# Kernel optimization log

Hardware: AMD Instinct MI355X
Metric: run time of the kernel (lower is better)

The kernel has to match this reference:

```python
import jax, jax.numpy as jnp
import numpy as np

N = 50_000       # nodes
E = 1_600_000    # edges (avg degree 32)
F_IN = 128       # input features
H = 32           # hidden channels (both GCNConv layers)
C = 16           # num classes


def setup_inputs() -> dict:
    key = jax.random.key(0)
    ks = jax.random.split(key, 6)
    x = jax.random.normal(ks[0], (N, F_IN), dtype=jnp.float32)
    edge_index = jax.random.randint(ks[1], (2, E), 0, N, dtype=jnp.int32)
    W1 = jax.random.normal(ks[2], (F_IN, H), dtype=jnp.float32) / np.float32(np.sqrt(F_IN))
    b1 = jnp.zeros((H,), jnp.float32)
    W2 = jax.random.normal(ks[3], (H, H), dtype=jnp.float32) / np.float32(np.sqrt(H))
    b2 = jnp.zeros((H,), jnp.float32)
    Wc = jax.random.normal(ks[4], (H, C), dtype=jnp.float32) / np.float32(np.sqrt(H))
    bc = jnp.zeros((C,), jnp.float32)
    return {"x": x, "edge_index": edge_index, "W1": W1, "b1": b1,
            "W2": W2, "b2": b2, "Wc": Wc, "bc": bc}


def _gcn_conv(x, W, b, src, dst, deg_inv_sqrt, n):
    """PyG GCNConv: xW, then D^{-1/2}(A+I)D^{-1/2} aggregation, then bias.

    src/dst already include self-loops; deg_inv_sqrt precomputed on dst.
    """
    xw = x @ W                                   # [N, H]
    norm = deg_inv_sqrt[src] * deg_inv_sqrt[dst]  # [E+N]
    msg = xw[src] * norm[:, None]                # gather + scale, [E+N, H]
    out = jax.ops.segment_sum(msg, dst, num_segments=n)  # scatter-add
    return out + b


def reference(x, edge_index, W1, b1, W2, b2, Wc, bc):
    n = x.shape[0]
    loops = jnp.arange(n, dtype=edge_index.dtype)
    src = jnp.concatenate([edge_index[0], loops])  # add self-loops
    dst = jnp.concatenate([edge_index[1], loops])
    # degree over destination column (edge weight 1), as PyG gcn_norm does
    deg = jax.ops.segment_sum(jnp.ones_like(dst, dtype=x.dtype), dst, num_segments=n)
    deg_inv_sqrt = jnp.where(deg > 0, jax.lax.rsqrt(deg), 0.0)

    h = jnp.tanh(_gcn_conv(x, W1, b1, src, dst, deg_inv_sqrt, n))
    h = jnp.tanh(_gcn_conv(h, W2, b2, src, dst, deg_inv_sqrt, n))
    out = h @ Wc + bc
    return (out, h)
```

## Files before the change

kernel.cpp:

```cpp
#include <hip/hip_runtime.h>
#include <hip/hip_bf16.h>

#define NN 50000
#define EE 1600000
#define FIN 128
#define HH 32
#define CC 16
#define NB 782
#define NBLK 782
#define CHUNK 2048
#define FCAP 3072

typedef unsigned short u16;
typedef unsigned int u32;
typedef unsigned char u8;

__device__ __forceinline__ float bf2f(u16 u) {
    union { u32 i; float f; } v; v.i = ((u32)u) << 16; return v.f;
}
__device__ __forceinline__ u16 f2bf(float f) {
    union { float f; u32 i; } v; v.f = f;
    u32 x = v.i;
    return (u16)((x + 0x7fffu + ((x >> 16) & 1u)) >> 16);
}

__global__ __launch_bounds__(256) void k_place(const int* __restrict__ src, const int* __restrict__ dst,
                                               int* __restrict__ locT,
                                               u16* __restrict__ gsrc, u8* __restrict__ grel) {
    __shared__ int dst_s[CHUNK];
    __shared__ u16 s_src[CHUNK];
    __shared__ u8  s_rel[CHUNK];
    __shared__ int cur[NB];
    __shared__ int ps[256];
    const int tid = threadIdx.x, blk = blockIdx.x;
    const int e0 = blk * CHUNK;
    int cnt = EE - e0; if (cnt > CHUNK) cnt = CHUNK;

    const uint4* gd4 = (const uint4*)(dst + e0);
    for (int i = tid; i < cnt / 4; i += 256) ((uint4*)dst_s)[i] = gd4[i];
    for (int i = tid; i < NB; i += 256) cur[i] = 0;
    __syncthreads();

    for (int k = 0; k < CHUNK / 256; ++k) {
        int i = k * 256 + tid;
        if (i < cnt) atomicAdd(&cur[dst_s[i] >> 6], 1);
    }
    __syncthreads();

    const int bi = tid * 4;
    int v0 = 0, v1 = 0, v2 = 0, v3 = 0;
    if (bi < NB)     v0 = cur[bi];
    if (bi + 1 < NB) v1 = cur[bi + 1];
    if (bi + 2 < NB) v2 = cur[bi + 2];
    if (bi + 3 < NB) v3 = cur[bi + 3];
    ps[tid] = v0 + v1 + v2 + v3;
    __syncthreads();
    for (int off = 1; off < 256; off <<= 1) {
        int t = (tid >= off) ? ps[tid - off] : 0;
        __syncthreads();
        ps[tid] += t;
        __syncthreads();
    }
    int run = (tid == 0) ? 0 : ps[tid - 1];
    if (bi < NB)     { cur[bi] = run;     locT[(size_t)bi * NBLK + blk] = run;       run += v0; }
    if (bi + 1 < NB) { cur[bi + 1] = run; locT[(size_t)(bi + 1) * NBLK + blk] = run; run += v1; }
    if (bi + 2 < NB) { cur[bi + 2] = run; locT[(size_t)(bi + 2) * NBLK + blk] = run; run += v2; }
    if (bi + 3 < NB) { cur[bi + 3] = run; locT[(size_t)(bi + 3) * NBLK + blk] = run; run += v3; }
    if (tid == 255) locT[(size_t)NB * NBLK + blk] = ps[255];
    __syncthreads();

    for (int k = 0; k < CHUNK / 256; ++k) {
        int i = k * 256 + tid;
        if (i < cnt) {
            int d = dst_s[i];
            int pos = atomicAdd(&cur[d >> 6], 1);
            s_src[pos] = (u16)src[e0 + i];
            s_rel[pos] = (u8)(d & 63);
        }
    }
    __syncthreads();

    const uint4* ss = (const uint4*)s_src;
    uint4* gs = (uint4*)(gsrc + (size_t)blk * CHUNK);
    for (int i = tid; i < (cnt * 2) / 16; i += 256) gs[i] = ss[i];
    const uint4* sr = (const uint4*)s_rel;
    uint4* gr = (uint4*)(grel + (size_t)blk * CHUNK);
    for (int i = tid; i < cnt / 16; i += 256) gr[i] = sr[i];
}

__global__ __launch_bounds__(256) void k_btot(const int* __restrict__ locT, int* __restrict__ btot) {
    __shared__ int ps[256];
    const int cb = blockIdx.x;
    int s = 0;
    for (int b = threadIdx.x; b < NBLK; b += 256)
        s += locT[(size_t)(cb + 1) * NBLK + b] - locT[(size_t)cb * NBLK + b];
    ps[threadIdx.x] = s;
    __syncthreads();
    for (int off = 128; off > 0; off >>= 1) {
        if (threadIdx.x < off) ps[threadIdx.x] += ps[threadIdx.x + off];
        __syncthreads();
    }
    if (threadIdx.x == 0) btot[cb] = ps[0];
}

__global__ __launch_bounds__(1024) void k_cscan(const int* __restrict__ btot, int* __restrict__ cbase,
                                                int* __restrict__ rowptr,
                                                const u32* __restrict__ xw_words, int* __restrict__ flag) {
    __shared__ int ps[1024];
    __shared__ int cs;
    const int t = threadIdx.x;
    if (t == 0) cs = 0;
    __syncthreads();
    if (t < 512) {
        float v = fabsf(bf2f((u16)(xw_words[t] & 0xffffu)));
        if (v >= 6.0e-8f && v <= 64.0f) atomicAdd(&cs, 1);
    }
    int myv = (t < NB) ? btot[t] : 0;
    ps[t] = myv;
    __syncthreads();
    for (int off = 1; off < 1024; off <<= 1) {
        int v = (t >= off) ? ps[t - off] : 0;
        __syncthreads();
        ps[t] += v;
        __syncthreads();
    }
    if (t < NB) cbase[t] = ps[t] - myv;
    if (t == 0) {
        cbase[NB] = EE; rowptr[NN] = EE;
        *flag = (cs > 384) ? 1 : 0;
    }
}

__global__ __launch_bounds__(256) void k_fine(const int* __restrict__ locT, const int* __restrict__ cbase,
                                              const u16* __restrict__ gsrc, const u8* __restrict__ grel,
                                              int* __restrict__ rowptr, float* __restrict__ dis,
                                              u16* __restrict__ entries) {
    __shared__ int beg_s[NBLK];
    __shared__ int fo[NBLK + 1];
    __shared__ int ps[256];
    __shared__ int h[64];
    __shared__ int cur[64];
    __shared__ u16 lsrc[FCAP];
    __shared__ u8  lrel[FCAP];
    __shared__ u16 lout[FCAP];
    const int tid = threadIdx.x, cb = blockIdx.x;

    for (int b = tid; b < NBLK; b += 256) {
        int beg = locT[(size_t)cb * NBLK + b];
        beg_s[b] = beg;
        fo[b] = locT[(size_t)(cb + 1) * NBLK + b] - beg;
    }
    if (tid < 64) h[tid] = 0;
    __syncthreads();

    const int b0 = tid * 4;
    int a0 = 0, a1 = 0, a2 = 0, a3 = 0;
    if (b0 < NBLK)     a0 = fo[b0];
    if (b0 + 1 < NBLK) a1 = fo[b0 + 1];
    if (b0 + 2 < NBLK) a2 = fo[b0 + 2];
    if (b0 + 3 < NBLK) a3 = fo[b0 + 3];
    ps[tid] = a0 + a1 + a2 + a3;
    __syncthreads();
    for (int off = 1; off < 256; off <<= 1) {
        int v = (tid >= off) ? ps[tid - off] : 0;
        __syncthreads();
        ps[tid] += v;
        __syncthreads();
    }
    int run = (tid == 0) ? 0 : ps[tid - 1];
    if (b0 < NBLK)     { fo[b0] = run;     run += a0; }
    if (b0 + 1 < NBLK) { fo[b0 + 1] = run; run += a1; }
    if (b0 + 2 < NBLK) { fo[b0 + 2] = run; run += a2; }
    if (b0 + 3 < NBLK) { fo[b0 + 3] = run; run += a3; }
    if (tid == 255) fo[NBLK] = ps[255];
    __syncthreads();
    const int T = fo[NBLK];
    const int base = cbase[cb];
    const bool staged = (T <= FCAP);

    if (staged) {
        for (int b = tid; b < NBLK; b += 256) {
            int g0 = b * CHUNK + beg_s[b];
            int o = fo[b];
            int L = fo[b + 1] - o;
            for (int j = 0; j < L; ++j) {
                u8 r = grel[g0 + j];
                lrel[o + j] = r;
                lsrc[o + j] = gsrc[g0 + j];
                atomicAdd(&h[r], 1);
            }
        }
    } else {
        for (int b = tid; b < NBLK; b += 256) {
            int g0 = b * CHUNK + beg_s[b];
            int L = fo[b + 1] - fo[b];
            for (int j = 0; j < L; ++j) atomicAdd(&h[grel[g0 + j]], 1);
        }
    }
    __syncthreads();

    int myv = (tid < 64) ? h[tid] : 0;
    ps[tid] = (tid < 64) ? myv : 0;
    __syncthreads();
    for (int off = 1; off < 64; off <<= 1) {
        int v = (tid >= off && tid < 64) ? ps[tid - off] : 0;
        __syncthreads();
        if (tid < 64) ps[tid] += v;
        __syncthreads();
    }
    if (tid < 64) {
        int excl = ps[tid] - myv;
        int n = cb * 64 + tid;
        cur[tid] = staged ? excl : base + excl;
        if (n < NN) {
            rowptr[n] = base + excl;
            dis[n] = rsqrtf((float)myv + 1.0f);
        }
    }
    __syncthreads();

    if (staged) {
        for (int i = tid; i < T; i += 256) {
            int pos = atomicAdd(&cur[lrel[i]], 1);
            lout[pos] = lsrc[i];
        }
        __syncthreads();
        for (int i = tid; i < T; i += 256) entries[base + i] = lout[i];
    } else {
        for (int b = tid; b < NBLK; b += 256) {
            int g0 = b * CHUNK + beg_s[b];
            int L = fo[b + 1] - fo[b];
            for (int j = 0; j < L; ++j) {
                int g = g0 + j;
                int pos = atomicAdd(&cur[grel[g]], 1);
                entries[pos] = gsrc[g];
            }
        }
    }
}

__global__ __launch_bounds__(256) void k_xw1(const void* __restrict__ xv, const void* __restrict__ W1v,
                                             const float* __restrict__ dis,
                                             const int* __restrict__ flag, u16* __restrict__ xwb) {
    __shared__ float wsm[FIN * HH];
    __shared__ float xs[128][33];
    const int f = *flag;
    const int tid = threadIdx.x;
    if (f) {
        const u16* W1 = (const u16*)W1v;
        for (int i = tid; i < FIN * HH; i += 256) wsm[i] = bf2f(W1[i]);
    } else {
        const float* W1 = (const float*)W1v;
        for (int i = tid; i < FIN * HH; i += 256) wsm[i] = W1[i];
    }
    const int n0 = blockIdx.x * 128;
    const int ct = tid & 7, rg = tid >> 3;
    const int lr = tid >> 1, lh = tid & 1;
    int ln = n0 + lr; if (ln >= NN) ln = NN - 1;
    float acc[4][4] = {};
    for (int kc = 0; kc < FIN; kc += 32) {
        __syncthreads();
        float* dq = &xs[lr][lh * 16];
        if (f) {
            const u16* lp = (const u16*)xv + (size_t)ln * FIN + lh * 16 + kc;
            uint4 a = *(const uint4*)lp;
            uint4 b = *(const uint4*)(lp + 8);
            u32 aw[4] = {a.x, a.y, a.z, a.w}, bw[4] = {b.x, b.y, b.z, b.w};
            #pragma unroll
            for (int i = 0; i < 4; ++i) {
                dq[2*i]     = bf2f((u16)(aw[i] & 0xffffu));
                dq[2*i+1]   = bf2f((u16)(aw[i] >> 16));
                dq[8+2*i]   = bf2f((u16)(bw[i] & 0xffffu));
                dq[8+2*i+1] = bf2f((u16)(bw[i] >> 16));
            }
        } else {
            const float* lp = (const float*)xv + (size_t)ln * FIN + lh * 16 + kc;
            #pragma unroll
            for (int i = 0; i < 4; ++i) {
                float4 t = *(const float4*)(lp + 4 * i);
                dq[4*i] = t.x; dq[4*i+1] = t.y; dq[4*i+2] = t.z; dq[4*i+3] = t.w;
            }
        }
        __syncthreads();
        #pragma unroll
        for (int k = 0; k < 32; ++k) {
            float4 wv = *(const float4*)&wsm[(kc + k) * HH + ct * 4];
            #pragma unroll
            for (int j = 0; j < 4; ++j) {
                float xvv = xs[rg * 4 + j][k];
                acc[j][0] = fmaf(xvv, wv.x, acc[j][0]);
                acc[j][1] = fmaf(xvv, wv.y, acc[j][1]);
                acc[j][2] = fmaf(xvv, wv.z, acc[j][2]);
                acc[j][3] = fmaf(xvv, wv.w, acc[j][3]);
            }
        }
    }
    #pragma unroll
    for (int j = 0; j < 4; ++j) {
        int n = n0 + rg * 4 + j;
        if (n < NN) {
            float dd = dis[n];
            ushort4 o;
            o.x = f2bf(dd * acc[j][0]); o.y = f2bf(dd * acc[j][1]);
            o.z = f2bf(dd * acc[j][2]); o.w = f2bf(dd * acc[j][3]);
            *(ushort4*)&xwb[(size_t)n * HH + ct * 4] = o;
        }
    }
}

__global__ __launch_bounds__(256) void k_xw2(const u16* __restrict__ h1, const void* __restrict__ W2v,
                                             const float* __restrict__ dis,
                                             const int* __restrict__ flag, u16* __restrict__ xwb) {
    __shared__ float wsm[HH * HH];
    __shared__ float xs[128][33];
    const int f = *flag;
    const int tid = threadIdx.x;
    if (f) {
        const u16* W2 = (const u16*)W2v;
        for (int i = tid; i < HH * HH; i += 256) wsm[i] = bf2f(W2[i]);
    } else {
        const float* W2 = (const float*)W2v;
        for (int i = tid; i < HH * HH; i += 256) wsm[i] = W2[i];
    }
    const int n0 = blockIdx.x * 128;
    const int lr = tid >> 1, lh = tid & 1;
    int ln = n0 + lr; if (ln >= NN) ln = NN - 1;
    const u16* lp = h1 + (size_t)ln * HH + lh * 16;
    uint4 a = *(const uint4*)lp;
    uint4 b = *(const uint4*)(lp + 8);
    float* dq = &xs[lr][lh * 16];
    u32 aw[4] = {a.x, a.y, a.z, a.w}, bw[4] = {b.x, b.y, b.z, b.w};
    #pragma unroll
    for (int i = 0; i < 4; ++i) {
        dq[2*i]     = bf2f((u16)(aw[i] & 0xffffu));
        dq[2*i+1]   = bf2f((u16)(aw[i] >> 16));
        dq[8+2*i]   = bf2f((u16)(bw[i] & 0xffffu));
        dq[8+2*i+1] = bf2f((u16)(bw[i] >> 16));
    }
    __syncthreads();
    const int ct = tid & 7, rg = tid >> 3;
    float acc[4][4] = {};
    #pragma unroll
    for (int k = 0; k < 32; ++k) {
        float4 wv = *(const float4*)&wsm[k * HH + ct * 4];
        #pragma unroll
        for (int j = 0; j < 4; ++j) {
            float xv = xs[rg * 4 + j][k];
            acc[j][0] = fmaf(xv, wv.x, acc[j][0]);
            acc[j][1] = fmaf(xv, wv.y, acc[j][1]);
            acc[j][2] = fmaf(xv, wv.z, acc[j][2]);
            acc[j][3] = fmaf(xv, wv.w, acc[j][3]);
        }
    }
    #pragma unroll
    for (int j = 0; j < 4; ++j) {
        int n = n0 + rg * 4 + j;
        if (n < NN) {
            float dd = dis[n];
            ushort4 o;
            o.x = f2bf(dd * acc[j][0]); o.y = f2bf(dd * acc[j][1]);
            o.z = f2bf(dd * acc[j][2]); o.w = f2bf(dd * acc[j][3]);
            *(ushort4*)&xwb[(size_t)n * HH + ct * 4] = o;
        }
    }
}

__global__ __launch_bounds__(256) void k_gather(const int* __restrict__ rowptr, const u16* __restrict__ entries,
                                                const u16* __restrict__ xws, const float* __restrict__ dis,
                                                const void* __restrict__ bv, const int* __restrict__ flag,
                                                int force16, u16* __restrict__ dst16, float* __restrict__ dst32,
                                                int do_cls, const void* __restrict__ Wcv,
                                                const void* __restrict__ bcv, void* __restrict__ outv) {
    __shared__ float hrow[16][32];
    __shared__ float wcs[HH * CC];
    __shared__ float bcs[CC];
    const int f = *flag;
    const int tid = threadIdx.x;
    if (do_cls) {
        if (f) {
            const u16* Wc = (const u16*)Wcv;
            for (int i = tid; i < HH * CC; i += 256) wcs[i] = bf2f(Wc[i]);
            if (tid < CC) bcs[tid] = bf2f(((const u16*)bcv)[tid]);
        } else {
            const float* Wc = (const float*)Wcv;
            for (int i = tid; i < HH * CC; i += 256) wcs[i] = Wc[i];
            if (tid < CC) bcs[tid] = ((const float*)bcv)[tid];
        }
    }
    const int nl = tid >> 4;
    const int g = blockIdx.x * 16 + nl;
    const int c0 = (tid & 15) * 2;
    float b0, b1;
    if (f) { b0 = bf2f(((const u16*)bv)[c0]); b1 = bf2f(((const u16*)bv)[c0 + 1]); }
    else   { b0 = ((const float*)bv)[c0];     b1 = ((const float*)bv)[c0 + 1]; }
    const int beg = rowptr[g], end = rowptr[g + 1];
    const float dd = dis[g];
    u32 sw = *(const u32*)&xws[(size_t)g * HH + c0];
    float aL0 = bf2f((u16)(sw & 0xffffu)), aH0 = bf2f((u16)(sw >> 16));
    float aL1 = 0.f, aH1 = 0.f, aL2 = 0.f, aH2 = 0.f, aL3 = 0.f, aH3 = 0.f;
    int i = beg;
    for (; i < end && (i & 3); ++i) {
        u32 w = *(const u32*)&xws[(size_t)entries[i] * HH + c0];
        aL0 += bf2f((u16)(w & 0xffffu)); aH0 += bf2f((u16)(w >> 16));
    }
    for (; i + 4 <= end; i += 4) {
        ushort4 e4 = *(const ushort4*)&entries[i];
        u32 w0 = *(const u32*)&xws[(size_t)e4.x * HH + c0];
        u32 w1 = *(const u32*)&xws[(size_t)e4.y * HH + c0];
        u32 w2 = *(const u32*)&xws[(size_t)e4.z * HH + c0];
        u32 w3 = *(const u32*)&xws[(size_t)e4.w * HH + c0];
        aL0 += bf2f((u16)(w0 & 0xffffu)); aH0 += bf2f((u16)(w0 >> 16));
        aL1 += bf2f((u16)(w1 & 0xffffu)); aH1 += bf2f((u16)(w1 >> 16));
        aL2 += bf2f((u16)(w2 & 0xffffu)); aH2 += bf2f((u16)(w2 >> 16));
        aL3 += bf2f((u16)(w3 & 0xffffu)); aH3 += bf2f((u16)(w3 >> 16));
    }
    for (; i < end; ++i) {
        u32 w = *(const u32*)&xws[(size_t)entries[i] * HH + c0];
        aL0 += bf2f((u16)(w & 0xffffu)); aH0 += bf2f((u16)(w >> 16));
    }
    float vLo = tanhf(fmaf(dd, (aL0 + aL1) + (aL2 + aL3), b0));
    float vHi = tanhf(fmaf(dd, (aH0 + aH1) + (aH2 + aH3), b1));
    size_t idx = (size_t)g * HH + c0;
    if (force16 | f) {
        u32 o = (u32)f2bf(vLo) | ((u32)f2bf(vHi) << 16);
        *(u32*)&dst16[idx] = o;
    } else {
        *(float2*)&dst32[idx] = make_float2(vLo, vHi);
    }
    if (do_cls) {
        hrow[nl][c0] = vLo; hrow[nl][c0 + 1] = vHi;
        __syncthreads();
        int cl = tid & 15;
        float acc = bcs[cl];
        #pragma unroll
        for (int k = 0; k < HH; ++k) acc = fmaf(hrow[nl][k], wcs[k * CC + cl], acc);
        size_t oi = (size_t)g * CC + cl;
        if (f) ((u16*)outv)[oi] = f2bf(acc);
        else   ((float*)outv)[oi] = acc;
    }
}

extern "C" void kernel_launch(void* const* d_in, const int* in_sizes, int n_in,
                              void* d_out, int out_size, void* d_ws, size_t ws_size,
                              hipStream_t stream) {
    const void* x  = d_in[0];
    const int*  ei = (const int*)d_in[1];
    const void* W1 = d_in[2];
    const void* b1 = d_in[3];
    const void* W2 = d_in[4];
    const void* b2 = d_in[5];
    const void* Wc = d_in[6];
    const void* bc = d_in[7];
    const int* srcv = ei;
    const int* dstv = ei + EE;

    char*  ws     = (char*)d_ws;
    int*   flag   = (int*)ws;
    int*   rowptr = (int*)(ws + 4096);
    float* dis    = (float*)(ws + 208896);
    int*   cbase  = (int*)(ws + 413696);
    int*   btot   = (int*)(ws + 417792);
    int*   locT   = (int*)(ws + 421888);
    u16*   xwb    = (u16*)(ws + 2871296);
    u16*   entries= (u16*)(ws + 6071296);

    u16*   gsrc = (u16*)d_out;
    u8*    grel = (u8*)d_out + (size_t)EE * 2;

    u16*   h1    = (u16*)d_out;
    u16*   h2_16 = (u16*)d_out + (size_t)NN * CC;
    float* h2_32 = (float*)d_out + (size_t)NN * CC;

    k_place<<<NBLK, 256, 0, stream>>>(srcv, dstv, locT, gsrc, grel);
    k_btot<<<NB, 256, 0, stream>>>(locT, btot);
    k_cscan<<<1, 1024, 0, stream>>>(btot, cbase, rowptr, (const u32*)x, flag);
    k_fine<<<NB, 256, 0, stream>>>(locT, cbase, gsrc, grel, rowptr, dis, entries);

    k_xw1<<<(NN + 127) / 128, 256, 0, stream>>>(x, W1, dis, flag, xwb);
    k_gather<<<NN / 16, 256, 0, stream>>>(rowptr, entries, xwb, dis, b1, flag,
                                          1, h1, (float*)nullptr,
                                          0, nullptr, nullptr, nullptr);

    k_xw2<<<(NN + 127) / 128, 256, 0, stream>>>(h1, W2, dis, flag, xwb);
    k_gather<<<NN / 16, 256, 0, stream>>>(rowptr, entries, xwb, dis, b2, flag,
                                          0, h2_16, h2_32,
                                          1, Wc, bc, d_out);
}
```

Baseline: 191.8 us.

## Fuse layer-2 matmul into layer-1 gather and drop the single-block scan kernel

Removes the k_cscan single-block kernel. Its prefix offset is now computed redundantly inside each k_fine block by summing btot over the preceding blocks, and the dtype-flag detection moves into block 0 of k_btot. The layer-1 gather now applies the W2 matmul and the deg^-1/2 scaling in-block and writes xw2 directly. This eliminates the separate k_xw2 kernel and the h1 round-trip through memory. The result is two fewer launches and less global traffic, at the cost of a per-block reduction over up to 782 ints in k_fine and an extra 32x32 FMA loop per node in the gather.

```diff
diff --git a/kernel.cpp b/kernel.cpp
--- a/kernel.cpp
+++ b/kernel.cpp
@@ -88,50 +88,36 @@
     for (int i = tid; i < cnt / 16; i += 256) gr[i] = sr[i];
 }
 
-__global__ __launch_bounds__(256) void k_btot(const int* __restrict__ locT, int* __restrict__ btot) {
+__global__ __launch_bounds__(256) void k_btot(const int* __restrict__ locT, int* __restrict__ btot,
+                                              const u32* __restrict__ xw_words, int* __restrict__ flag) {
     __shared__ int ps[256];
-    const int cb = blockIdx.x;
+    __shared__ int cs;
+    const int tid = threadIdx.x, cb = blockIdx.x;
+    if (cb == 0) {
+        if (tid == 0) cs = 0;
+        __syncthreads();
+        int c = 0;
+        for (int i = tid; i < 512; i += 256) {
+            float v = fabsf(bf2f((u16)(xw_words[i] & 0xffffu)));
+            if (v >= 6.0e-8f && v <= 64.0f) c++;
+        }
+        atomicAdd(&cs, c);
+        __syncthreads();
+        if (tid == 0) *flag = (cs > 384) ? 1 : 0;
+    }
     int s = 0;
-    for (int b = threadIdx.x; b < NBLK; b += 256)
+    for (int b = tid; b < NBLK; b += 256)
         s += locT[(size_t)(cb + 1) * NBLK + b] - locT[(size_t)cb * NBLK + b];
-    ps[threadIdx.x] = s;
+    ps[tid] = s;
     __syncthreads();
     for (int off = 128; off > 0; off >>= 1) {
-        if (threadIdx.x < off) ps[threadIdx.x] += ps[threadIdx.x + off];
-        __syncthreads();
-    }
-    if (threadIdx.x == 0) btot[cb] = ps[0];
-}
-
-__global__ __launch_bounds__(1024) void k_cscan(const int* __restrict__ btot, int* __restrict__ cbase,
-                                                int* __restrict__ rowptr,
-                                                const u32* __restrict__ xw_words, int* __restrict__ flag) {
-    __shared__ int ps[1024];
-    __shared__ int cs;
-    const int t = threadIdx.x;
-    if (t == 0) cs = 0;
-    __syncthreads();
-    if (t < 512) {
-        float v = fabsf(bf2f((u16)(xw_words[t] & 0xffffu)));
-        if (v >= 6.0e-8f && v <= 64.0f) atomicAdd(&cs, 1);
-    }
-    int myv = (t < NB) ? btot[t] : 0;
-    ps[t] = myv;
-    __syncthreads();
-    for (int off = 1; off < 1024; off <<= 1) {
-        int v = (t >= off) ? ps[t - off] : 0;
-        __syncthreads();
-        ps[t] += v;
-        __syncthreads();
-    }
-    if (t < NB) cbase[t] = ps[t] - myv;
-    if (t == 0) {
-        cbase[NB] = EE; rowptr[NN] = EE;
-        *flag = (cs > 384) ? 1 : 0;
-    }
-}
-
-__global__ __launch_bounds__(256) void k_fine(const int* __restrict__ locT, const int* __restrict__ cbase,
+        if (tid < off) ps[tid] += ps[tid + off];
+        __syncthreads();
+    }
+    if (tid == 0) btot[cb] = ps[0];
+}
+
+__global__ __launch_bounds__(256) void k_fine(const int* __restrict__ locT, const int* __restrict__ btot,
                                               const u16* __restrict__ gsrc, const u8* __restrict__ grel,
                                               int* __restrict__ rowptr, float* __restrict__ dis,
                                               u16* __restrict__ entries) {
@@ -140,6 +126,7 @@
     __shared__ int ps[256];
     __shared__ int h[64];
     __shared__ int cur[64];
+    __shared__ int sbase;
     __shared__ u16 lsrc[FCAP];
     __shared__ u8  lrel[FCAP];
     __shared__ u16 lout[FCAP];
@@ -151,7 +138,18 @@
         fo[b] = locT[(size_t)(cb + 1) * NBLK + b] - beg;
     }
     if (tid < 64) h[tid] = 0;
-    __syncthreads();
+
+    int bs = 0;
+    for (int j = tid; j < cb; j += 256) bs += btot[j];
+    ps[tid] = bs;
+    __syncthreads();
+    for (int off = 128; off > 0; off >>= 1) {
+        if (tid < off) ps[tid] += ps[tid + off];
+        __syncthreads();
+    }
+    if (tid == 0) sbase = ps[0];
+    __syncthreads();
+    const int base = sbase;
 
     const int b0 = tid * 4;
     int a0 = 0, a1 = 0, a2 = 0, a3 = 0;
@@ -175,7 +173,6 @@
     if (tid == 255) fo[NBLK] = ps[255];
     __syncthreads();
     const int T = fo[NBLK];
-    const int base = cbase[cb];
     const bool staged = (T <= FCAP);
 
     if (staged) {
@@ -217,6 +214,7 @@
             dis[n] = rsqrtf((float)myv + 1.0f);
         }
     }
+    if (cb == NB - 1 && tid == 0) rowptr[NN] = EE;
     __syncthreads();
 
     if (staged) {
@@ -308,84 +306,20 @@
     }
 }
 
-__global__ __launch_bounds__(256) void k_xw2(const u16* __restrict__ h1, const void* __restrict__ W2v,
-                                             const float* __restrict__ dis,
-                                             const int* __restrict__ flag, u16* __restrict__ xwb) {
-    __shared__ float wsm[HH * HH];
-    __shared__ float xs[128][33];
+__global__ __launch_bounds__(256) void k_g1(const int* __restrict__ rowptr, const u16* __restrict__ entries,
+                                            const u16* __restrict__ xws, const float* __restrict__ dis,
+                                            const void* __restrict__ bv, const int* __restrict__ flag,
+                                            const void* __restrict__ W2v, u16* __restrict__ xwb2) {
+    __shared__ float hrow[16][32];
+    __shared__ float w2s[HH * HH];
     const int f = *flag;
     const int tid = threadIdx.x;
     if (f) {
         const u16* W2 = (const u16*)W2v;
-        for (int i = tid; i < HH * HH; i += 256) wsm[i] = bf2f(W2[i]);
+        for (int i = tid; i < HH * HH; i += 256) w2s[i] = bf2f(W2[i]);
     } else {
         const float* W2 = (const float*)W2v;
-        for (int i = tid; i < HH * HH; i += 256) wsm[i] = W2[i];
-    }
-    const int n0 = blockIdx.x * 128;
-    const int lr = tid >> 1, lh = tid & 1;
-    int ln = n0 + lr; if (ln >= NN) ln = NN - 1;
-    const u16* lp = h1 + (size_t)ln * HH + lh * 16;
-    uint4 a = *(const uint4*)lp;
-    uint4 b = *(const uint4*)(lp + 8);
-    float* dq = &xs[lr][lh * 16];
-    u32 aw[4] = {a.x, a.y, a.z, a.w}, bw[4] = {b.x, b.y, b.z, b.w};
-    #pragma unroll
-    for (int i = 0; i < 4; ++i) {
-        dq[2*i]     = bf2f((u16)(aw[i] & 0xffffu));
-        dq[2*i+1]   = bf2f((u16)(aw[i] >> 16));
-        dq[8+2*i]   = bf2f((u16)(bw[i] & 0xffffu));
-        dq[8+2*i+1] = bf2f((u16)(bw[i] >> 16));
-    }
-    __syncthreads();
-    const int ct = tid & 7, rg = tid >> 3;
-    float acc[4][4] = {};
-    #pragma unroll
-    for (int k = 0; k < 32; ++k) {
-        float4 wv = *(const float4*)&wsm[k * HH + ct * 4];
-        #pragma unroll
-        for (int j = 0; j < 4; ++j) {
-            float xv = xs[rg * 4 + j][k];
-            acc[j][0] = fmaf(xv, wv.x, acc[j][0]);
-            acc[j][1] = fmaf(xv, wv.y, acc[j][1]);
-            acc[j][2] = fmaf(xv, wv.z, acc[j][2]);
-            acc[j][3] = fmaf(xv, wv.w, acc[j][3]);
-        }
-    }
-    #pragma unroll
-    for (int j = 0; j < 4; ++j) {
-        int n = n0 + rg * 4 + j;
-        if (n < NN) {
-            float dd = dis[n];
-            ushort4 o;
-            o.x = f2bf(dd * acc[j][0]); o.y = f2bf(dd * acc[j][1]);
-            o.z = f2bf(dd * acc[j][2]); o.w = f2bf(dd * acc[j][3]);
-            *(ushort4*)&xwb[(size_t)n * HH + ct * 4] = o;
-        }
-    }
-}
-
-__global__ __launch_bounds__(256) void k_gather(const int* __restrict__ rowptr, const u16* __restrict__ entries,
-                                                const u16* __restrict__ xws, const float* __restrict__ dis,
-                                                const void* __restrict__ bv, const int* __restrict__ flag,
-                                                int force16, u16* __restrict__ dst16, float* __restrict__ dst32,
-                                                int do_cls, const void* __restrict__ Wcv,
-                                                const void* __restrict__ bcv, void* __restrict__ outv) {
-    __shared__ float hrow[16][32];
-    __shared__ float wcs[HH * CC];
-    __shared__ float bcs[CC];
-    const int f = *flag;
-    const int tid = threadIdx.x;
-    if (do_cls) {
-        if (f) {
-            const u16* Wc = (const u16*)Wcv;
-            for (int i = tid; i < HH * CC; i += 256) wcs[i] = bf2f(Wc[i]);
-            if (tid < CC) bcs[tid] = bf2f(((const u16*)bcv)[tid]);
-        } else {
-            const float* Wc = (const float*)Wcv;
-            for (int i = tid; i < HH * CC; i += 256) wcs[i] = Wc[i];
-            if (tid < CC) bcs[tid] = ((const float*)bcv)[tid];
-        }
+        for (int i = tid; i < HH * HH; i += 256) w2s[i] = W2[i];
     }
     const int nl = tid >> 4;
     const int g = blockIdx.x * 16 + nl;
@@ -420,24 +354,89 @@
     }
     float vLo = tanhf(fmaf(dd, (aL0 + aL1) + (aL2 + aL3), b0));
     float vHi = tanhf(fmaf(dd, (aH0 + aH1) + (aH2 + aH3), b1));
+    hrow[nl][c0] = vLo; hrow[nl][c0 + 1] = vHi;
+    __syncthreads();
+    float a0 = 0.f, a1 = 0.f;
+    #pragma unroll
+    for (int k = 0; k < HH; ++k) {
+        float hv = hrow[nl][k];
+        a0 = fmaf(hv, w2s[k * HH + c0], a0);
+        a1 = fmaf(hv, w2s[k * HH + c0 + 1], a1);
+    }
+    u32 o = (u32)f2bf(dd * a0) | ((u32)f2bf(dd * a1) << 16);
+    *(u32*)&xwb2[(size_t)g * HH + c0] = o;
+}
+
+__global__ __launch_bounds__(256) void k_g2(const int* __restrict__ rowptr, const u16* __restrict__ entries,
+                                            const u16* __restrict__ xws, const float* __restrict__ dis,
+                                            const void* __restrict__ bv, const int* __restrict__ flag,
+                                            const void* __restrict__ Wcv, const void* __restrict__ bcv,
+                                            void* __restrict__ outbase) {
+    __shared__ float hrow[16][32];
+    __shared__ float wcs[HH * CC];
+    __shared__ float bcs[CC];
+    const int f = *flag;
+    const int tid = threadIdx.x;
+    if (f) {
+        const u16* Wc = (const u16*)Wcv;
+        for (int i = tid; i < HH * CC; i += 256) wcs[i] = bf2f(Wc[i]);
+        if (tid < CC) bcs[tid] = bf2f(((const u16*)bcv)[tid]);
+    } else {
+        const float* Wc = (const float*)Wcv;
+        for (int i = tid; i < HH * CC; i += 256) wcs[i] = Wc[i];
+        if (tid < CC) bcs[tid] = ((const float*)bcv)[tid];
+    }
+    const int nl = tid >> 4;
+    const int g = blockIdx.x * 16 + nl;
+    const int c0 = (tid & 15) * 2;
+    float b0, b1;
+    if (f) { b0 = bf2f(((const u16*)bv)[c0]); b1 = bf2f(((const u16*)bv)[c0 + 1]); }
+    else   { b0 = ((const float*)bv)[c0];     b1 = ((const float*)bv)[c0 + 1]; }
+    const int beg = rowptr[g], end = rowptr[g + 1];
+    const float dd = dis[g];
+    u32 sw = *(const u32*)&xws[(size_t)g * HH + c0];
+    float aL0 = bf2f((u16)(sw & 0xffffu)), aH0 = bf2f((u16)(sw >> 16));
+    float aL1 = 0.f, aH1 = 0.f, aL2 = 0.f, aH2 = 0.f, aL3 = 0.f, aH3 = 0.f;
+    int i = beg;
+    for (; i < end && (i & 3); ++i) {
+        u32 w = *(const u32*)&xws[(size_t)entries[i] * HH + c0];
+        aL0 += bf2f((u16)(w & 0xffffu)); aH0 += bf2f((u16)(w >> 16));
+    }
+    for (; i + 4 <= end; i += 4) {
+        ushort4 e4 = *(const ushort4*)&entries[i];
+        u32 w0 = *(const u32*)&xws[(size_t)e4.x * HH + c0];
+        u32 w1 = *(const u32*)&xws[(size_t)e4.y * HH + c0];
+        u32 w2 = *(const u32*)&xws[(size_t)e4.z * HH + c0];
+        u32 w3 = *(const u32*)&xws[(size_t)e4.w * HH + c0];
+        aL0 += bf2f((u16)(w0 & 0xffffu)); aH0 += bf2f((u16)(w0 >> 16));
+        aL1 += bf2f((u16)(w1 & 0xffffu)); aH1 += bf2f((u16)(w1 >> 16));
+        aL2 += bf2f((u16)(w2 & 0xffffu)); aH2 += bf2f((u16)(w2 >> 16));
+        aL3 += bf2f((u16)(w3 & 0xffffu)); aH3 += bf2f((u16)(w3 >> 16));
+    }
+    for (; i < end; ++i) {
+        u32 w = *(const u32*)&xws[(size_t)entries[i] * HH + c0];
+        aL0 += bf2f((u16)(w & 0xffffu)); aH0 += bf2f((u16)(w >> 16));
+    }
+    float vLo = tanhf(fmaf(dd, (aL0 + aL1) + (aL2 + aL3), b0));
+    float vHi = tanhf(fmaf(dd, (aH0 + aH1) + (aH2 + aH3), b1));
     size_t idx = (size_t)g * HH + c0;
-    if (force16 | f) {
+    if (f) {
+        u16* h2_16 = (u16*)outbase + (size_t)NN * CC;
         u32 o = (u32)f2bf(vLo) | ((u32)f2bf(vHi) << 16);
-        *(u32*)&dst16[idx] = o;
-    } else {
-        *(float2*)&dst32[idx] = make_float2(vLo, vHi);
-    }
-    if (do_cls) {
-        hrow[nl][c0] = vLo; hrow[nl][c0 + 1] = vHi;
-        __syncthreads();
-        int cl = tid & 15;
-        float acc = bcs[cl];
-        #pragma unroll
-        for (int k = 0; k < HH; ++k) acc = fmaf(hrow[nl][k], wcs[k * CC + cl], acc);
-        size_t oi = (size_t)g * CC + cl;
-        if (f) ((u16*)outv)[oi] = f2bf(acc);
-        else   ((float*)outv)[oi] = acc;
-    }
+        *(u32*)&h2_16[idx] = o;
+    } else {
+        float* h2_32 = (float*)outbase + (size_t)NN * CC;
+        *(float2*)&h2_32[idx] = make_float2(vLo, vHi);
+    }
+    hrow[nl][c0] = vLo; hrow[nl][c0 + 1] = vHi;
+    __syncthreads();
+    int cl = tid & 15;
+    float acc = bcs[cl];
+    #pragma unroll
+    for (int k = 0; k < HH; ++k) acc = fmaf(hrow[nl][k], wcs[k * CC + cl], acc);
+    size_t oi = (size_t)g * CC + cl;
+    if (f) ((u16*)outbase)[oi] = f2bf(acc);
+    else   ((float*)outbase)[oi] = acc;
 }
 
 extern "C" void kernel_launch(void* const* d_in, const int* in_sizes, int n_in,
@@ -458,31 +457,20 @@
     int*   flag   = (int*)ws;
     int*   rowptr = (int*)(ws + 4096);
     float* dis    = (float*)(ws + 208896);
-    int*   cbase  = (int*)(ws + 413696);
     int*   btot   = (int*)(ws + 417792);
     int*   locT   = (int*)(ws + 421888);
     u16*   xwb    = (u16*)(ws + 2871296);
     u16*   entries= (u16*)(ws + 6071296);
+    u16*   xwb2   = (u16*)(ws + 9271296);
 
     u16*   gsrc = (u16*)d_out;
     u8*    grel = (u8*)d_out + (size_t)EE * 2;
 
-    u16*   h1    = (u16*)d_out;
-    u16*   h2_16 = (u16*)d_out + (size_t)NN * CC;
-    float* h2_32 = (float*)d_out + (size_t)NN * CC;
-
     k_place<<<NBLK, 256, 0, stream>>>(srcv, dstv, locT, gsrc, grel);
-    k_btot<<<NB, 256, 0, stream>>>(locT, btot);
-    k_cscan<<<1, 1024, 0, stream>>>(btot, cbase, rowptr, (const u32*)x, flag);
-    k_fine<<<NB, 256, 0, stream>>>(locT, cbase, gsrc, grel, rowptr, dis, entries);
+    k_btot<<<NB, 256, 0, stream>>>(locT, btot, (const u32*)x, flag);
+    k_fine<<<NB, 256, 0, stream>>>(locT, btot, gsrc, grel, rowptr, dis, entries);
 
     k_xw1<<<(NN + 127) / 128, 256, 0, stream>>>(x, W1, dis, flag, xwb);
-    k_gather<<<NN / 16, 256, 0, stream>>>(rowptr, entries, xwb, dis, b1, flag,
-                                          1, h1, (float*)nullptr,
-                                          0, nullptr, nullptr, nullptr);
-
-    k_xw2<<<(NN + 127) / 128, 256, 0, stream>>>(h1, W2, dis, flag, xwb);
-    k_gather<<<NN / 16, 256, 0, stream>>>(rowptr, entries, xwb, dis, b2, flag,
-                                          0, h2_16, h2_32,
-                                          1, Wc, bc, d_out);
-}
+    k_g1<<<NN / 16, 256, 0, stream>>>(rowptr, entries, xwb, dis, b1, flag, W2, xwb2);
+    k_g2<<<NN / 16, 256, 0, stream>>>(rowptr, entries, xwb2, dis, b2, flag, Wc, bc, d_out);
+}
```

After: 185.8 us. -3.2%, faster.
